# Kernel tuning notes

Measured on AMD Instinct MI355X. Metric: run time of the kernel, lower is better.

Reference implementation:

```python
import jax, jax.numpy as jnp
import numpy as np

B, N, C = 64, 900, 16
NCHAR, L = 75, 8
K_CLASS, K_L1, K_GIOU, K_STRING = 1.0, 5.0, 2.0, 10.0


def _pointwise_giou(p, t):
    # p, t: [..., 4] xyxy valid boxes. Elementwise GIoU == diagonal of pairwise GIoU.
    lt = jnp.maximum(p[..., :2], t[..., :2])
    rb = jnp.minimum(p[..., 2:], t[..., 2:])
    wh = jnp.clip(rb - lt, 0.0)
    inter = wh[..., 0] * wh[..., 1]
    area_p = (p[..., 2] - p[..., 0]) * (p[..., 3] - p[..., 1])
    area_t = (t[..., 2] - t[..., 0]) * (t[..., 3] - t[..., 1])
    union = area_p + area_t - inter
    iou = inter / union
    lt_c = jnp.minimum(p[..., :2], t[..., :2])
    rb_c = jnp.maximum(p[..., 2:], t[..., 2:])
    wh_c = jnp.clip(rb_c - lt_c, 0.0)
    area_c = wh_c[..., 0] * wh_c[..., 1]
    return iou - (area_c - union) / area_c


def setup_inputs() -> dict:
    key = jax.random.key(0)
    k1, k2, k3, k4, k5, k6, k7 = jax.random.split(key, 7)
    pred_logits = jax.random.normal(k1, (B, N, C), dtype=jnp.float32)
    pred_boxes = jax.random.uniform(k2, (B, N, 8), dtype=jnp.float32)
    pred_string_logits = jax.random.normal(k3, (B, NCHAR, N, L), dtype=jnp.float32)
    # valid xyxy GT boxes in [0,1]
    xy1 = jax.random.uniform(k4, (B, 2), dtype=jnp.float32) * 0.5
    wh = jax.random.uniform(k5, (B, 2), dtype=jnp.float32) * 0.5 + 1e-3
    tgt_bboxes = jnp.concatenate([xy1, xy1 + wh], axis=-1)
    plate_type = jax.random.randint(k6, (B,), 0, C, dtype=jnp.int64)
    lps = jax.random.randint(k7, (B, L), 0, NCHAR, dtype=jnp.int64)
    return {"pred_logits": pred_logits, "pred_boxes": pred_boxes,
            "pred_string_logits": pred_string_logits, "tgt_bboxes": tgt_bboxes,
            "plate_type": plate_type, "lps": lps}


def reference(pred_logits, pred_boxes, pred_string_logits, tgt_bboxes, plate_type, lps):
    # class cost: -softmax prob of target class per image
    out_prob = jax.nn.softmax(pred_logits, axis=-1)                      # [B,N,C]
    cost_class = -jnp.take_along_axis(out_prob, plate_type[:, None, None], axis=-1)[..., 0]  # [B,N]

    # vertices -> axis-aligned xyxy
    verts = pred_boxes.reshape(B, N, 4, 2)
    pred_xyxy = jnp.concatenate([verts.min(axis=2), verts.max(axis=2)], axis=-1)  # [B,N,4]

    # L1 bbox cost (cdist p=1 against the single target per image)
    cost_bbox = jnp.abs(pred_xyxy - tgt_bboxes[:, None, :]).sum(-1)      # [B,N]

    # GIoU cost (pointwise == diagonal of the original pairwise matrix)
    cost_giou = -_pointwise_giou(pred_xyxy, tgt_bboxes[:, None, :])       # [B,N]

    # string CE cost: logits [B,n_char,N,L], targets lps[B,L]
    logp = jax.nn.log_softmax(pred_string_logits, axis=1)                # [B,n_char,N,L]
    idx = jnp.broadcast_to(lps[:, None, None, :L], (B, 1, N, L))
    ce = -jnp.take_along_axis(logp, idx, axis=1)[:, 0]                   # [B,N,L]
    cost_string = ce.mean(axis=-1)                                       # [B,N]

    Cmat = (K_CLASS * cost_class + K_L1 * cost_bbox
            + K_GIOU * cost_giou + K_STRING * cost_string)               # [B,N]
    return jnp.argmin(Cmat, axis=1, keepdims=True)                       # [B,1]
```

## Files before the change

### kernel.cpp

```cpp
#include <hip/hip_runtime.h>

#define B_ 64
#define N_ 900
#define C_ 16
#define NCHAR_ 75
#define L_ 8

__global__ __launch_bounds__(64) void cost_kernel(
    const float* __restrict__ logits,
    const float* __restrict__ boxes,
    const float* __restrict__ ps,
    const float* __restrict__ tgt,
    const int*   __restrict__ ptype,
    const int*   __restrict__ lps,
    float* __restrict__ cost)
{
    int idx = blockIdx.x * 64 + threadIdx.x;
    if (idx >= B_ * N_) return;
    int b = idx / N_;
    int n = idx - b * N_;

    int tl[L_];
    {
        const int4* lp4 = (const int4*)(lps + b * L_);
        int4 q0 = lp4[0], q1 = lp4[1];
        tl[0]=q0.x; tl[1]=q0.y; tl[2]=q0.z; tl[3]=q0.w;
        tl[4]=q1.x; tl[5]=q1.y; tl[6]=q1.z; tl[7]=q1.w;
    }
    float s[L_], tv[L_];
    #pragma unroll
    for (int l = 0; l < L_; ++l) { s[l] = 0.0f; tv[l] = 0.0f; }

    const float* base = ps + ((size_t)b * NCHAR_ * N_ + n) * L_;
    #pragma unroll 5
    for (int c = 0; c < NCHAR_; ++c) {
        const float4* p4 = (const float4*)(base + (size_t)c * (N_ * L_));
        float4 a = p4[0];
        float4 d = p4[1];
        float v0 = a.x, v1 = a.y, v2 = a.z, v3 = a.w;
        float v4 = d.x, v5 = d.y, v6 = d.z, v7 = d.w;
        s[0] += __expf(v0); tv[0] = (c == tl[0]) ? v0 : tv[0];
        s[1] += __expf(v1); tv[1] = (c == tl[1]) ? v1 : tv[1];
        s[2] += __expf(v2); tv[2] = (c == tl[2]) ? v2 : tv[2];
        s[3] += __expf(v3); tv[3] = (c == tl[3]) ? v3 : tv[3];
        s[4] += __expf(v4); tv[4] = (c == tl[4]) ? v4 : tv[4];
        s[5] += __expf(v5); tv[5] = (c == tl[5]) ? v5 : tv[5];
        s[6] += __expf(v6); tv[6] = (c == tl[6]) ? v6 : tv[6];
        s[7] += __expf(v7); tv[7] = (c == tl[7]) ? v7 : tv[7];
    }
    float ce = 0.0f;
    #pragma unroll
    for (int l = 0; l < L_; ++l) ce += __logf(s[l]) - tv[l];
    float cost_string = ce * (1.0f / L_);

    float x[C_];
    {
        const float4* lg = (const float4*)(logits + (size_t)idx * C_);
        float4 q0 = lg[0], q1 = lg[1], q2 = lg[2], q3 = lg[3];
        x[0]=q0.x; x[1]=q0.y; x[2]=q0.z; x[3]=q0.w;
        x[4]=q1.x; x[5]=q1.y; x[6]=q1.z; x[7]=q1.w;
        x[8]=q2.x; x[9]=q2.y; x[10]=q2.z; x[11]=q2.w;
        x[12]=q3.x; x[13]=q3.y; x[14]=q3.z; x[15]=q3.w;
    }
    int tcls = ptype[b];
    float m = x[0];
    #pragma unroll
    for (int i = 1; i < C_; ++i) m = fmaxf(m, x[i]);
    float se = 0.0f, xt = 0.0f;
    #pragma unroll
    for (int i = 0; i < C_; ++i) {
        se += __expf(x[i] - m);
        xt = (i == tcls) ? x[i] : xt;
    }
    float cost_class = -__expf(xt - m) / se;

    float4 tb = *(const float4*)(tgt + b * 4);
    const float4* bx = (const float4*)(boxes + (size_t)idx * 8);
    float4 w0 = bx[0], w1 = bx[1];
    float px1 = fminf(fminf(w0.x, w0.z), fminf(w1.x, w1.z));
    float py1 = fminf(fminf(w0.y, w0.w), fminf(w1.y, w1.w));
    float px2 = fmaxf(fmaxf(w0.x, w0.z), fmaxf(w1.x, w1.z));
    float py2 = fmaxf(fmaxf(w0.y, w0.w), fmaxf(w1.y, w1.w));

    float cost_bbox = fabsf(px1 - tb.x) + fabsf(py1 - tb.y)
                    + fabsf(px2 - tb.z) + fabsf(py2 - tb.w);

    float ltx = fmaxf(px1, tb.x), lty = fmaxf(py1, tb.y);
    float rbx = fminf(px2, tb.z), rby = fminf(py2, tb.w);
    float iw = fmaxf(rbx - ltx, 0.0f), ih = fmaxf(rby - lty, 0.0f);
    float inter = iw * ih;
    float area_p = (px2 - px1) * (py2 - py1);
    float area_t = (tb.z - tb.x) * (tb.w - tb.y);
    float uni = area_p + area_t - inter;
    float iou = inter / uni;
    float cx1 = fminf(px1, tb.x), cy1 = fminf(py1, tb.y);
    float cx2 = fmaxf(px2, tb.z), cy2 = fmaxf(py2, tb.w);
    float cw = fmaxf(cx2 - cx1, 0.0f), ch = fmaxf(cy2 - cy1, 0.0f);
    float area_c = cw * ch;
    float giou = iou - (area_c - uni) / area_c;

    cost[idx] = cost_class + 5.0f * cost_bbox - 2.0f * giou + 10.0f * cost_string;
}

__global__ __launch_bounds__(256) void argmin_kernel(
    const float* __restrict__ cost, int* __restrict__ out)
{
    int b = blockIdx.x;
    int t = threadIdx.x;
    const float* cb = cost + b * N_;
    float bv = 3.4e38f;
    int bi = 0;
    for (int n = t; n < N_; n += 256) {
        float v = cb[n];
        if (v < bv) { bv = v; bi = n; }
    }
    __shared__ float sv[256];
    __shared__ int   si[256];
    sv[t] = bv; si[t] = bi;
    __syncthreads();
    for (int off = 128; off > 0; off >>= 1) {
        if (t < off) {
            float v2 = sv[t + off]; int i2 = si[t + off];
            if (v2 < sv[t] || (v2 == sv[t] && i2 < si[t])) { sv[t] = v2; si[t] = i2; }
        }
        __syncthreads();
    }
    if (t == 0) out[b] = si[0];
}

extern "C" void kernel_launch(void* const* d_in, const int* in_sizes, int n_in,
                              void* d_out, int out_size, void* d_ws, size_t ws_size,
                              hipStream_t stream) {
    const float* logits = (const float*)d_in[0];
    const float* boxes  = (const float*)d_in[1];
    const float* ps     = (const float*)d_in[2];
    const float* tgt    = (const float*)d_in[3];
    const int*   ptype  = (const int*)d_in[4];
    const int*   lps    = (const int*)d_in[5];

    float* cost = (float*)d_ws;
    int*   out  = (int*)d_out;

    cost_kernel<<<(B_ * N_ + 63) / 64, 64, 0, stream>>>(
        logits, boxes, ps, tgt, ptype, lps, cost);
    argmin_kernel<<<B_, 256, 0, stream>>>(cost, out);
}
```

Baseline: 30.13 us.

## Split each query across eight lanes, one per string position, with shuffle reductions

Result: slower. 31.07 us (+3.1%).

```diff
diff --git a/kernel.cpp b/kernel.cpp
--- a/kernel.cpp
+++ b/kernel.cpp
@@ -6,7 +6,7 @@
 #define NCHAR_ 75
 #define L_ 8
 
-__global__ __launch_bounds__(64) void cost_kernel(
+__global__ __launch_bounds__(256) void cost_kernel(
     const float* __restrict__ logits,
     const float* __restrict__ boxes,
     const float* __restrict__ ps,
@@ -15,73 +15,56 @@
     const int*   __restrict__ lps,
     float* __restrict__ cost)
 {
-    int idx = blockIdx.x * 64 + threadIdx.x;
-    if (idx >= B_ * N_) return;
-    int b = idx / N_;
-    int n = idx - b * N_;
+    int tid = blockIdx.x * 256 + threadIdx.x;
+    int l  = tid & 7;
+    int bn = tid >> 3;
+    int b  = bn / N_;
+    int n  = bn - b * N_;
+    int lane = threadIdx.x & 63;
 
-    int tl[L_];
-    {
-        const int4* lp4 = (const int4*)(lps + b * L_);
-        int4 q0 = lp4[0], q1 = lp4[1];
-        tl[0]=q0.x; tl[1]=q0.y; tl[2]=q0.z; tl[3]=q0.w;
-        tl[4]=q1.x; tl[5]=q1.y; tl[6]=q1.z; tl[7]=q1.w;
+    int tl = lps[b * L_ + l];
+    const float* p = ps + ((size_t)b * NCHAR_ * N_ + n) * L_ + l;
+    float s = 0.0f, tv = 0.0f;
+    #pragma unroll
+    for (int c = 0; c < NCHAR_; ++c) {
+        float v = p[(size_t)c * (N_ * L_)];
+        s += __expf(v);
+        tv = (c == tl) ? v : tv;
     }
-    float s[L_], tv[L_];
-    #pragma unroll
-    for (int l = 0; l < L_; ++l) { s[l] = 0.0f; tv[l] = 0.0f; }
+    float part = __logf(s) - tv;
+    part += __shfl_xor(part, 1);
+    part += __shfl_xor(part, 2);
+    part += __shfl_xor(part, 4);
+    float cost_string = part * (1.0f / L_);
 
-    const float* base = ps + ((size_t)b * NCHAR_ * N_ + n) * L_;
-    #pragma unroll 5
-    for (int c = 0; c < NCHAR_; ++c) {
-        const float4* p4 = (const float4*)(base + (size_t)c * (N_ * L_));
-        float4 a = p4[0];
-        float4 d = p4[1];
-        float v0 = a.x, v1 = a.y, v2 = a.z, v3 = a.w;
-        float v4 = d.x, v5 = d.y, v6 = d.z, v7 = d.w;
-        s[0] += __expf(v0); tv[0] = (c == tl[0]) ? v0 : tv[0];
-        s[1] += __expf(v1); tv[1] = (c == tl[1]) ? v1 : tv[1];
-        s[2] += __expf(v2); tv[2] = (c == tl[2]) ? v2 : tv[2];
-        s[3] += __expf(v3); tv[3] = (c == tl[3]) ? v3 : tv[3];
-        s[4] += __expf(v4); tv[4] = (c == tl[4]) ? v4 : tv[4];
-        s[5] += __expf(v5); tv[5] = (c == tl[5]) ? v5 : tv[5];
-        s[6] += __expf(v6); tv[6] = (c == tl[6]) ? v6 : tv[6];
-        s[7] += __expf(v7); tv[7] = (c == tl[7]) ? v7 : tv[7];
-    }
-    float ce = 0.0f;
-    #pragma unroll
-    for (int l = 0; l < L_; ++l) ce += __logf(s[l]) - tv[l];
-    float cost_string = ce * (1.0f / L_);
+    float2 xy = ((const float2*)(logits + (size_t)bn * C_))[l];
+    float a = xy.x, bvl = xy.y;
+    float m = fmaxf(a, bvl);
+    m = fmaxf(m, __shfl_xor(m, 1));
+    m = fmaxf(m, __shfl_xor(m, 2));
+    m = fmaxf(m, __shfl_xor(m, 4));
+    float ea = __expf(a - m), eb = __expf(bvl - m);
+    float se = ea + eb;
+    se += __shfl_xor(se, 1);
+    se += __shfl_xor(se, 2);
+    se += __shfl_xor(se, 4);
+    int tcls = ptype[b];
+    float xe = (tcls == 2 * l) ? ea : ((tcls == 2 * l + 1) ? eb : 0.0f);
+    xe += __shfl_xor(xe, 1);
+    xe += __shfl_xor(xe, 2);
+    xe += __shfl_xor(xe, 4);
+    float cost_class = -xe / se;
 
-    float x[C_];
-    {
-        const float4* lg = (const float4*)(logits + (size_t)idx * C_);
-        float4 q0 = lg[0], q1 = lg[1], q2 = lg[2], q3 = lg[3];
-        x[0]=q0.x; x[1]=q0.y; x[2]=q0.z; x[3]=q0.w;
-        x[4]=q1.x; x[5]=q1.y; x[6]=q1.z; x[7]=q1.w;
-        x[8]=q2.x; x[9]=q2.y; x[10]=q2.z; x[11]=q2.w;
-        x[12]=q3.x; x[13]=q3.y; x[14]=q3.z; x[15]=q3.w;
-    }
-    int tcls = ptype[b];
-    float m = x[0];
-    #pragma unroll
-    for (int i = 1; i < C_; ++i) m = fmaxf(m, x[i]);
-    float se = 0.0f, xt = 0.0f;
-    #pragma unroll
-    for (int i = 0; i < C_; ++i) {
-        se += __expf(x[i] - m);
-        xt = (i == tcls) ? x[i] : xt;
-    }
-    float cost_class = -__expf(xt - m) / se;
+    float v  = boxes[(size_t)bn * 8 + l];
+    float mn = fminf(v, __shfl_xor(v, 2));  mn = fminf(mn, __shfl_xor(mn, 4));
+    float mx = fmaxf(v, __shfl_xor(v, 2));  mx = fmaxf(mx, __shfl_xor(mx, 4));
+    int grp = lane & ~7;
+    float px1 = __shfl(mn, grp + 0);
+    float py1 = __shfl(mn, grp + 1);
+    float px2 = __shfl(mx, grp + 0);
+    float py2 = __shfl(mx, grp + 1);
 
     float4 tb = *(const float4*)(tgt + b * 4);
-    const float4* bx = (const float4*)(boxes + (size_t)idx * 8);
-    float4 w0 = bx[0], w1 = bx[1];
-    float px1 = fminf(fminf(w0.x, w0.z), fminf(w1.x, w1.z));
-    float py1 = fminf(fminf(w0.y, w0.w), fminf(w1.y, w1.w));
-    float px2 = fmaxf(fmaxf(w0.x, w0.z), fmaxf(w1.x, w1.z));
-    float py2 = fmaxf(fmaxf(w0.y, w0.w), fmaxf(w1.y, w1.w));
-
     float cost_bbox = fabsf(px1 - tb.x) + fabsf(py1 - tb.y)
                     + fabsf(px2 - tb.z) + fabsf(py2 - tb.w);
 
@@ -99,7 +82,8 @@
     float area_c = cw * ch;
     float giou = iou - (area_c - uni) / area_c;
 
-    cost[idx] = cost_class + 5.0f * cost_bbox - 2.0f * giou + 10.0f * cost_string;
+    if (l == 0)
+        cost[bn] = cost_class + 5.0f * cost_bbox - 2.0f * giou + 10.0f * cost_string;
 }
 
 __global__ __launch_bounds__(256) void argmin_kernel(
@@ -141,7 +125,7 @@
     float* cost = (float*)d_ws;
     int*   out  = (int*)d_out;
 
-    cost_kernel<<<(B_ * N_ + 63) / 64, 64, 0, stream>>>(
+    cost_kernel<<<(B_ * N_ * L_) / 256, 256, 0, stream>>>(
         logits, boxes, ps, tgt, ptype, lps, cost);
     argmin_kernel<<<B_, 256, 0, stream>>>(cost, out);
 }
```

## Fuse cost computation and per-image argmin using packed 64-bit atomicMin

Applied to the files above, without the earlier changes.

Measured after the change: 35.61 us. 1.18x slower.

```diff
diff --git a/kernel.cpp b/kernel.cpp
--- a/kernel.cpp
+++ b/kernel.cpp
@@ -6,126 +6,132 @@
 #define NCHAR_ 75
 #define L_ 8
 
-__global__ __launch_bounds__(64) void cost_kernel(
+__global__ __launch_bounds__(256) void fused_kernel(
     const float* __restrict__ logits,
     const float* __restrict__ boxes,
     const float* __restrict__ ps,
     const float* __restrict__ tgt,
     const int*   __restrict__ ptype,
     const int*   __restrict__ lps,
-    float* __restrict__ cost)
+    unsigned long long* __restrict__ packed,
+    unsigned*           __restrict__ counter,
+    int* __restrict__ out)
 {
-    int idx = blockIdx.x * 64 + threadIdx.x;
-    if (idx >= B_ * N_) return;
-    int b = idx / N_;
-    int n = idx - b * N_;
+    int b     = blockIdx.x >> 2;
+    int chunk = blockIdx.x & 3;
+    int t     = threadIdx.x;
+    int n     = chunk * 225 + t;
+    bool active = (t < 225);
 
-    int tl[L_];
-    {
-        const int4* lp4 = (const int4*)(lps + b * L_);
-        int4 q0 = lp4[0], q1 = lp4[1];
-        tl[0]=q0.x; tl[1]=q0.y; tl[2]=q0.z; tl[3]=q0.w;
-        tl[4]=q1.x; tl[5]=q1.y; tl[6]=q1.z; tl[7]=q1.w;
+    unsigned long long pk = ~0ull;
+    if (active) {
+        int bn = b * N_ + n;
+
+        int tl[L_];
+        {
+            const int4* lp4 = (const int4*)(lps + b * L_);
+            int4 q0 = lp4[0], q1 = lp4[1];
+            tl[0]=q0.x; tl[1]=q0.y; tl[2]=q0.z; tl[3]=q0.w;
+            tl[4]=q1.x; tl[5]=q1.y; tl[6]=q1.z; tl[7]=q1.w;
+        }
+        float s[L_], tv[L_];
+        #pragma unroll
+        for (int l = 0; l < L_; ++l) { s[l] = 0.0f; tv[l] = 0.0f; }
+
+        const float* base = ps + ((size_t)b * NCHAR_ * N_ + n) * L_;
+        #pragma unroll 5
+        for (int c = 0; c < NCHAR_; ++c) {
+            const float4* p4 = (const float4*)(base + (size_t)c * (N_ * L_));
+            float4 a = p4[0];
+            float4 d = p4[1];
+            s[0] += __expf(a.x); tv[0] = (c == tl[0]) ? a.x : tv[0];
+            s[1] += __expf(a.y); tv[1] = (c == tl[1]) ? a.y : tv[1];
+            s[2] += __expf(a.z); tv[2] = (c == tl[2]) ? a.z : tv[2];
+            s[3] += __expf(a.w); tv[3] = (c == tl[3]) ? a.w : tv[3];
+            s[4] += __expf(d.x); tv[4] = (c == tl[4]) ? d.x : tv[4];
+            s[5] += __expf(d.y); tv[5] = (c == tl[5]) ? d.y : tv[5];
+            s[6] += __expf(d.z); tv[6] = (c == tl[6]) ? d.z : tv[6];
+            s[7] += __expf(d.w); tv[7] = (c == tl[7]) ? d.w : tv[7];
+        }
+        float ce = 0.0f;
+        #pragma unroll
+        for (int l = 0; l < L_; ++l) ce += __logf(s[l]) - tv[l];
+        float cost_string = ce * (1.0f / L_);
+
+        float x[C_];
+        {
+            const float4* lg = (const float4*)(logits + (size_t)bn * C_);
+            float4 q0 = lg[0], q1 = lg[1], q2 = lg[2], q3 = lg[3];
+            x[0]=q0.x; x[1]=q0.y; x[2]=q0.z; x[3]=q0.w;
+            x[4]=q1.x; x[5]=q1.y; x[6]=q1.z; x[7]=q1.w;
+            x[8]=q2.x; x[9]=q2.y; x[10]=q2.z; x[11]=q2.w;
+            x[12]=q3.x; x[13]=q3.y; x[14]=q3.z; x[15]=q3.w;
+        }
+        int tcls = ptype[b];
+        float m = x[0];
+        #pragma unroll
+        for (int i = 1; i < C_; ++i) m = fmaxf(m, x[i]);
+        float se = 0.0f, xt = 0.0f;
+        #pragma unroll
+        for (int i = 0; i < C_; ++i) {
+            se += __expf(x[i] - m);
+            xt = (i == tcls) ? x[i] : xt;
+        }
+        float cost_class = -__expf(xt - m) / se;
+
+        float4 tb = *(const float4*)(tgt + b * 4);
+        const float4* bx = (const float4*)(boxes + (size_t)bn * 8);
+        float4 w0 = bx[0], w1 = bx[1];
+        float px1 = fminf(fminf(w0.x, w0.z), fminf(w1.x, w1.z));
+        float py1 = fminf(fminf(w0.y, w0.w), fminf(w1.y, w1.w));
+        float px2 = fmaxf(fmaxf(w0.x, w0.z), fmaxf(w1.x, w1.z));
+        float py2 = fmaxf(fmaxf(w0.y, w0.w), fmaxf(w1.y, w1.w));
+
+        float cost_bbox = fabsf(px1 - tb.x) + fabsf(py1 - tb.y)
+                        + fabsf(px2 - tb.z) + fabsf(py2 - tb.w);
+
+        float ltx = fmaxf(px1, tb.x), lty = fmaxf(py1, tb.y);
+        float rbx = fminf(px2, tb.z), rby = fminf(py2, tb.w);
+        float iw = fmaxf(rbx - ltx, 0.0f), ih = fmaxf(rby - lty, 0.0f);
+        float inter = iw * ih;
+        float area_p = (px2 - px1) * (py2 - py1);
+        float area_t = (tb.z - tb.x) * (tb.w - tb.y);
+        float uni = area_p + area_t - inter;
+        float iou = inter / uni;
+        float cx1 = fminf(px1, tb.x), cy1 = fminf(py1, tb.y);
+        float cx2 = fmaxf(px2, tb.z), cy2 = fmaxf(py2, tb.w);
+        float cw = fmaxf(cx2 - cx1, 0.0f), ch = fmaxf(cy2 - cy1, 0.0f);
+        float area_c = cw * ch;
+        float giou = iou - (area_c - uni) / area_c;
+
+        float cost = cost_class + 5.0f * cost_bbox - 2.0f * giou + 10.0f * cost_string;
+
+        unsigned u = __float_as_uint(cost);
+        u = (u & 0x80000000u) ? ~u : (u | 0x80000000u);
+        pk = ((unsigned long long)u << 32) | (unsigned)n;
     }
-    float s[L_], tv[L_];
+
+    __shared__ unsigned long long sp[256];
+    sp[t] = pk;
+    __syncthreads();
     #pragma unroll
-    for (int l = 0; l < L_; ++l) { s[l] = 0.0f; tv[l] = 0.0f; }
-
-    const float* base = ps + ((size_t)b * NCHAR_ * N_ + n) * L_;
-    #pragma unroll 5
-    for (int c = 0; c < NCHAR_; ++c) {
-        const float4* p4 = (const float4*)(base + (size_t)c * (N_ * L_));
-        float4 a = p4[0];
-        float4 d = p4[1];
-        float v0 = a.x, v1 = a.y, v2 = a.z, v3 = a.w;
-        float v4 = d.x, v5 = d.y, v6 = d.z, v7 = d.w;
-        s[0] += __expf(v0); tv[0] = (c == tl[0]) ? v0 : tv[0];
-        s[1] += __expf(v1); tv[1] = (c == tl[1]) ? v1 : tv[1];
-        s[2] += __expf(v2); tv[2] = (c == tl[2]) ? v2 : tv[2];
-        s[3] += __expf(v3); tv[3] = (c == tl[3]) ? v3 : tv[3];
-        s[4] += __expf(v4); tv[4] = (c == tl[4]) ? v4 : tv[4];
-        s[5] += __expf(v5); tv[5] = (c == tl[5]) ? v5 : tv[5];
-        s[6] += __expf(v6); tv[6] = (c == tl[6]) ? v6 : tv[6];
-        s[7] += __expf(v7); tv[7] = (c == tl[7]) ? v7 : tv[7];
-    }
-    float ce = 0.0f;
-    #pragma unroll
-    for (int l = 0; l < L_; ++l) ce += __logf(s[l]) - tv[l];
-    float cost_string = ce * (1.0f / L_);
-
-    float x[C_];
-    {
-        const float4* lg = (const float4*)(logits + (size_t)idx * C_);
-        float4 q0 = lg[0], q1 = lg[1], q2 = lg[2], q3 = lg[3];
-        x[0]=q0.x; x[1]=q0.y; x[2]=q0.z; x[3]=q0.w;
-        x[4]=q1.x; x[5]=q1.y; x[6]=q1.z; x[7]=q1.w;
-        x[8]=q2.x; x[9]=q2.y; x[10]=q2.z; x[11]=q2.w;
-        x[12]=q3.x; x[13]=q3.y; x[14]=q3.z; x[15]=q3.w;
-    }
-    int tcls = ptype[b];
-    float m = x[0];
-    #pragma unroll
-    for (int i = 1; i < C_; ++i) m = fmaxf(m, x[i]);
-    float se = 0.0f, xt = 0.0f;
-    #pragma unroll
-    for (int i = 0; i < C_; ++i) {
-        se += __expf(x[i] - m);
-        xt = (i == tcls) ? x[i] : xt;
-    }
-    float cost_class = -__expf(xt - m) / se;
-
-    float4 tb = *(const float4*)(tgt + b * 4);
-    const float4* bx = (const float4*)(boxes + (size_t)idx * 8);
-    float4 w0 = bx[0], w1 = bx[1];
-    float px1 = fminf(fminf(w0.x, w0.z), fminf(w1.x, w1.z));
-    float py1 = fminf(fminf(w0.y, w0.w), fminf(w1.y, w1.w));
-    float px2 = fmaxf(fmaxf(w0.x, w0.z), fmaxf(w1.x, w1.z));
-    float py2 = fmaxf(fmaxf(w0.y, w0.w), fmaxf(w1.y, w1.w));
-
-    float cost_bbox = fabsf(px1 - tb.x) + fabsf(py1 - tb.y)
-                    + fabsf(px2 - tb.z) + fabsf(py2 - tb.w);
-
-    float ltx = fmaxf(px1, tb.x), lty = fmaxf(py1, tb.y);
-    float rbx = fminf(px2, tb.z), rby = fminf(py2, tb.w);
-    float iw = fmaxf(rbx - ltx, 0.0f), ih = fmaxf(rby - lty, 0.0f);
-    float inter = iw * ih;
-    float area_p = (px2 - px1) * (py2 - py1);
-    float area_t = (tb.z - tb.x) * (tb.w - tb.y);
-    float uni = area_p + area_t - inter;
-    float iou = inter / uni;
-    float cx1 = fminf(px1, tb.x), cy1 = fminf(py1, tb.y);
-    float cx2 = fmaxf(px2, tb.z), cy2 = fmaxf(py2, tb.w);
-    float cw = fmaxf(cx2 - cx1, 0.0f), ch = fmaxf(cy2 - cy1, 0.0f);
-    float area_c = cw * ch;
-    float giou = iou - (area_c - uni) / area_c;
-
-    cost[idx] = cost_class + 5.0f * cost_bbox - 2.0f * giou + 10.0f * cost_string;
-}
-
-__global__ __launch_bounds__(256) void argmin_kernel(
-    const float* __restrict__ cost, int* __restrict__ out)
-{
-    int b = blockIdx.x;
-    int t = threadIdx.x;
-    const float* cb = cost + b * N_;
-    float bv = 3.4e38f;
-    int bi = 0;
-    for (int n = t; n < N_; n += 256) {
-        float v = cb[n];
-        if (v < bv) { bv = v; bi = n; }
-    }
-    __shared__ float sv[256];
-    __shared__ int   si[256];
-    sv[t] = bv; si[t] = bi;
-    __syncthreads();
     for (int off = 128; off > 0; off >>= 1) {
         if (t < off) {
-            float v2 = sv[t + off]; int i2 = si[t + off];
-            if (v2 < sv[t] || (v2 == sv[t] && i2 < si[t])) { sv[t] = v2; si[t] = i2; }
+            unsigned long long o = sp[t + off];
+            if (o < sp[t]) sp[t] = o;
         }
         __syncthreads();
     }
-    if (t == 0) out[b] = si[0];
+
+    if (t == 0) {
+        atomicMin(&packed[b], sp[0]);
+        __threadfence();
+        unsigned old = atomicAdd(&counter[b], 1u);
+        if (old == 2u) {
+            unsigned long long v = atomicAdd(&packed[b], 0ull);
+            out[b] = (int)(v & 0xFFFFFFFFull);
+        }
+    }
 }
 
 extern "C" void kernel_launch(void* const* d_in, const int* in_sizes, int n_in,
@@ -138,10 +144,12 @@
     const int*   ptype  = (const int*)d_in[4];
     const int*   lps    = (const int*)d_in[5];
 
-    float* cost = (float*)d_ws;
-    int*   out  = (int*)d_out;
+    unsigned long long* packed  = (unsigned long long*)d_ws;
+    unsigned*           counter = (unsigned*)((char*)d_ws + 512);
+    int* out = (int*)d_out;
 
-    cost_kernel<<<(B_ * N_ + 63) / 64, 64, 0, stream>>>(
-        logits, boxes, ps, tgt, ptype, lps, cost);
-    argmin_kernel<<<B_, 256, 0, stream>>>(cost, out);
+    hipMemsetAsync(d_ws, 0xFF, 768, stream);
+
+    fused_kernel<<<256, 256, 0, stream>>>(
+        logits, boxes, ps, tgt, ptype, lps, packed, counter, out);
 }
```
